# Optimization experiments

Measured on AMD Instinct MI355X. Metric: run time of the kernel, lower is better.

## Reference

```python
import jax, jax.numpy as jnp
import numpy as np

COMM_RANGE = 0.5
PATCH = 32
B, N, C_IN, H, W = 32, 8, 3, 224, 224
C, S, HM, CO = 384, 49, 512, 256


def setup_inputs() -> dict:
    key = jax.random.key(0)
    ks = jax.random.split(key, 20)
    sc = 0.02
    return {
        "img_raw": jax.random.normal(ks[0], (B, N, C_IN, H, W), jnp.float32),
        "pos": jax.random.uniform(ks[1], (B, N, 3), jnp.float32),
        "rot": jax.random.uniform(ks[2], (B, N, 3), jnp.float32),
        "W_patch": jax.random.normal(ks[3], (C, C_IN, PATCH, PATCH), jnp.float32) * sc,
        "b_patch": jax.random.normal(ks[4], (C,), jnp.float32) * sc,
        "W1a": jax.random.normal(ks[5], (C, HM), jnp.float32) * sc,
        "W1b": jax.random.normal(ks[6], (C, HM), jnp.float32) * sc,
        "b1": jax.random.normal(ks[7], (HM,), jnp.float32) * sc,
        "W2": jax.random.normal(ks[8], (HM, CO), jnp.float32) * sc,
        "b2": jax.random.normal(ks[9], (CO,), jnp.float32) * sc,
        "Wp": jax.random.normal(ks[10], (CO, 2), jnp.float32) * sc,
        "bp": jax.random.normal(ks[11], (2,), jnp.float32) * sc,
        "Wpv": jax.random.normal(ks[12], (CO, 2), jnp.float32) * sc,
        "bpv": jax.random.normal(ks[13], (2,), jnp.float32) * sc,
        "Wr": jax.random.normal(ks[14], (CO, 2), jnp.float32) * sc,
        "br": jax.random.normal(ks[15], (2,), jnp.float32) * sc,
        "Wrv": jax.random.normal(ks[16], (CO, 1), jnp.float32) * sc,
        "brv": jax.random.normal(ks[17], (1,), jnp.float32) * sc,
    }


def reference(img_raw, pos, rot, W_patch, b_patch, W1a, W1b, b1, W2, b2,
              Wp, bp, Wpv, bpv, Wr, br, Wrv, brv):
    # enc: patch-embed all B*N node images ONCE (the original redundantly
    # re-encodes per edge; math per node is identical).
    img = img_raw.reshape(B * N, C_IN, H, W)
    x = jax.lax.conv_general_dilated(
        img, W_patch, window_strides=(PATCH, PATCH), padding='VALID',
        dimension_numbers=('NCHW', 'OIHW', 'NCHW'))          # [BN, C, 7, 7]
    feats = x.reshape(B * N, C, S).transpose(0, 2, 1) + b_patch  # [BN, S, C]
    feats = feats.reshape(B, N, S, C)

    # radius graph per batch (dense, fixed shape, masked) -- loop=False
    pos2 = pos[..., :2]                                      # [B, N, 2]
    d2 = jnp.sum((pos2[:, :, None] - pos2[:, None, :]) ** 2, axis=-1)
    mask = (d2 < COMM_RANGE ** 2) & (~jnp.eye(N, dtype=bool))  # [B, N, N]
    mf = mask.reshape(B * N * N).astype(feats.dtype)

    # msg: per-token MLP on concat(x_i, x_j); split first layer so we never
    # materialize the [B,N,N,S,2C] concat.
    a = jnp.einsum('bnsc,ch->bnsh', feats, W1a)              # receiver term
    g = jnp.einsum('bnsc,ch->bnsh', feats, W1b)              # sender term
    h = jax.nn.relu(a[:, :, None] + g[:, None, :] + b1)      # [B,N,N,S,HM]
    m = jnp.einsum('bijsh,ho->bijo', h / S, W2) + b2         # mean-pool + fc

    # post: four heads -> pos(2), pos_var(2), rot(2), rot_var(1)
    heads = jnp.concatenate(
        [m @ Wp + bp, m @ Wpv + bpv, m @ Wr + br, m @ Wrv + brv], axis=-1)
    edge_out = heads.reshape(B * N * N, 7) * mf[:, None]     # masked edges

    node_preds = jnp.zeros((B, N, 1, 60, 60), jnp.float32)
    return edge_out, mask.reshape(B * N * N), node_preds
```

## Files before the change

kernel.cpp:

```cpp
#include <hip/hip_runtime.h>
#include <hip/hip_bf16.h>

typedef __attribute__((ext_vector_type(4))) float f32x4;
typedef __attribute__((ext_vector_type(8))) short s16x8;
typedef unsigned short u16;
typedef unsigned int u32;

__device__ inline u16 f2bf(float f) {
    union { float f; u32 u; } v; v.f = f;
    u32 r = v.u + 0x7FFFu + ((v.u >> 16) & 1u);
    return (u16)(r >> 16);
}
__device__ inline float bfbits2f(u32 hi_bits) {
    union { u32 u; float f; } v; v.u = hi_bits; return v.f;
}

__global__ __launch_bounds__(256) void prep_w(
    const float* __restrict__ W_patch, u16* __restrict__ wpb,
    const float* __restrict__ W1a, const float* __restrict__ W1b,
    u16* __restrict__ w1cat,
    const float* __restrict__ W2, const float* __restrict__ b2,
    const float* __restrict__ Wp, const float* __restrict__ bp,
    const float* __restrict__ Wpv, const float* __restrict__ bpv,
    const float* __restrict__ Wr, const float* __restrict__ br,
    const float* __restrict__ Wrv, const float* __restrict__ brv,
    float* __restrict__ W2h, float* __restrict__ bias7) {
    const int NW = 147456;
    const int NC = 1024 * 384;
    const int NH = 3591;
    const int total = NW + NC + NH;
    for (int idx = blockIdx.x * 256 + threadIdx.x; idx < total; idx += 256 * 256) {
        if (idx < NW) {
            int i = idx * 8;
            s16x8 o;
#pragma unroll
            for (int q = 0; q < 8; q++) o[q] = (short)f2bf(W_patch[i + q]);
            *(s16x8*)(wpb + i) = o;
        } else if (idx < NW + NC) {
            int w = idx - NW;
            int h = w / 384, k = w - h * 384;
            float v = (h < 512) ? W1a[k * 512 + h] : W1b[k * 512 + (h - 512)];
            w1cat[w] = f2bf(v);
        } else {
            int w = idx - NW - NC;
            if (w < 3584) {
                int h = w / 7, kk = w - h * 7;
                float s = 0.f;
                for (int o = 0; o < 256; o++) {
                    float ww = (kk < 2) ? Wp[o * 2 + kk]
                             : (kk < 4) ? Wpv[o * 2 + kk - 2]
                             : (kk < 6) ? Wr[o * 2 + kk - 4]
                                        : Wrv[o];
                    s += W2[h * 256 + o] * ww;
                }
                W2h[w] = s;
            } else {
                int kk = w - 3584;
                float s = (kk < 2) ? bp[kk] : (kk < 4) ? bpv[kk - 2]
                        : (kk < 6) ? br[kk - 4] : brv[0];
                for (int o = 0; o < 256; o++) {
                    float ww = (kk < 2) ? Wp[o * 2 + kk]
                             : (kk < 4) ? Wpv[o * 2 + kk - 2]
                             : (kk < 6) ? Wr[o * 2 + kk - 4]
                                        : Wrv[o];
                    s += b2[o] * ww;
                }
                bias7[kk] = s;
            }
        }
    }
}

__global__ __launch_bounds__(256) void gemm1_im2col(
    const float* __restrict__ img, const u16* __restrict__ Bt,
    u16* __restrict__ Cb, const float* __restrict__ bias) {
    constexpr int K = 3072, N = 384;
    __shared__ __align__(16) u16 As[128 * 64];
    __shared__ __align__(16) u16 Bs[64 * 64];
    const int tid = threadIdx.x;
    const int wave = tid >> 6, lane = tid & 63;
    const int wr = wave >> 1, wc = wave & 1;
    const int row0 = blockIdx.x * 128, col0 = blockIdx.y * 64;
    const int lr = lane >> 3;
    const int lcb = (lane & 7) * 8;

    const float* abase[4];
    int arow[4];
#pragma unroll
    for (int q = 0; q < 4; q++) {
        int ch = q * 4 + wave;
        int rA = ch * 8 + lr;
        int m = row0 + rA;
        int n = m / 49, s = m - n * 49;
        int py = s / 7, px = s - py * 7;
        abase[q] = img + ((size_t)(n * 3) * 224 + py * 32) * 224 + px * 32;
        arow[q] = rA;
    }
    f32x4 acc[4][2] = {};

    for (int k0 = 0; k0 < K; k0 += 64) {
        __syncthreads();
#pragma unroll
        for (int q = 0; q < 2; q++) {
            int ch = q * 4 + wave;
            const u16* gB = Bt + (size_t)(col0 + ch * 8 + lr) * K + k0 + lcb;
            __builtin_amdgcn_global_load_lds(
                (const __attribute__((address_space(1))) unsigned int*)gB,
                (__attribute__((address_space(3))) unsigned int*)(Bs + ch * 512), 16, 0, 0);
        }
        const int k = k0 + lcb;
        const int c = k >> 10;
        const int r = (k & 1023) >> 5;
        const int cc = k & 31;
        const int koff = (c * 224 + r) * 224 + cc;
        float4 va[4], vb[4];
#pragma unroll
        for (int q = 0; q < 4; q++) {
            const float* src = abase[q] + koff;
            va[q] = *(const float4*)src;
            vb[q] = *(const float4*)(src + 4);
        }
#pragma unroll
        for (int q = 0; q < 4; q++) {
            s16x8 o;
            o[0] = (short)f2bf(va[q].x); o[1] = (short)f2bf(va[q].y);
            o[2] = (short)f2bf(va[q].z); o[3] = (short)f2bf(va[q].w);
            o[4] = (short)f2bf(vb[q].x); o[5] = (short)f2bf(vb[q].y);
            o[6] = (short)f2bf(vb[q].z); o[7] = (short)f2bf(vb[q].w);
            *(s16x8*)(As + arow[q] * 64 + lcb) = o;
        }
        __syncthreads();
#pragma unroll
        for (int kk = 0; kk < 64; kk += 32) {
            s16x8 af[4], bfr[2];
#pragma unroll
            for (int m = 0; m < 4; m++)
                af[m] = *(const s16x8*)(As + (wr * 64 + m * 16 + (lane & 15)) * 64 + kk + (lane >> 4) * 8);
#pragma unroll
            for (int n = 0; n < 2; n++)
                bfr[n] = *(const s16x8*)(Bs + (wc * 32 + n * 16 + (lane & 15)) * 64 + kk + (lane >> 4) * 8);
#pragma unroll
            for (int m = 0; m < 4; m++)
#pragma unroll
                for (int n = 0; n < 2; n++)
                    acc[m][n] = __builtin_amdgcn_mfma_f32_16x16x32_bf16(af[m], bfr[n], acc[m][n], 0, 0, 0);
        }
    }
#pragma unroll
    for (int m = 0; m < 4; m++) {
        int drow = row0 + wr * 64 + m * 16 + (lane >> 4) * 4;
#pragma unroll
        for (int n = 0; n < 2; n++) {
            int dcol = col0 + wc * 32 + n * 16 + (lane & 15);
            float bv = bias[dcol];
#pragma unroll
            for (int i = 0; i < 4; i++)
                Cb[(size_t)(drow + i) * N + dcol] = f2bf(acc[m][n][i] + bv);
        }
    }
}

template<int BM, int BN>
__global__ __launch_bounds__(256) void gemm_bt(const u16* __restrict__ A,
                                               const u16* __restrict__ Bt,
                                               u16* __restrict__ Cb,
                                               const float* __restrict__ bias,
                                               int M, int N, int K) {
    constexpr int MF = BM / 32;
    constexpr int NF = BN / 32;
    __shared__ __align__(16) u16 As[BM * 64];
    __shared__ __align__(16) u16 Bs[BN * 64];
    const int tid = threadIdx.x;
    const int wave = tid >> 6, lane = tid & 63;
    const int wr = wave >> 1, wc = wave & 1;
    const int row0 = blockIdx.x * BM, col0 = blockIdx.y * BN;
    const int lr = lane >> 3;
    const int lcb = (lane & 7) * 8;
    f32x4 acc[MF][NF] = {};

    for (int k0 = 0; k0 < K; k0 += 64) {
        __syncthreads();
#pragma unroll
        for (int q = 0; q < BM / 32; q++) {
            int ch = q * 4 + wave;
            const u16* gA = A + (size_t)(row0 + ch * 8 + lr) * K + k0 + lcb;
            __builtin_amdgcn_global_load_lds(
                (const __attribute__((address_space(1))) unsigned int*)gA,
                (__attribute__((address_space(3))) unsigned int*)(As + ch * 512), 16, 0, 0);
        }
#pragma unroll
        for (int q = 0; q < BN / 32; q++) {
            int ch = q * 4 + wave;
            const u16* gB = Bt + (size_t)(col0 + ch * 8 + lr) * K + k0 + lcb;
            __builtin_amdgcn_global_load_lds(
                (const __attribute__((address_space(1))) unsigned int*)gB,
                (__attribute__((address_space(3))) unsigned int*)(Bs + ch * 512), 16, 0, 0);
        }
        __syncthreads();
#pragma unroll
        for (int kk = 0; kk < 64; kk += 32) {
            s16x8 af[MF], bfr[NF];
#pragma unroll
            for (int m = 0; m < MF; m++)
                af[m] = *(const s16x8*)(As + (wr * (BM / 2) + m * 16 + (lane & 15)) * 64 + kk + (lane >> 4) * 8);
#pragma unroll
            for (int n = 0; n < NF; n++)
                bfr[n] = *(const s16x8*)(Bs + (wc * (BN / 2) + n * 16 + (lane & 15)) * 64 + kk + (lane >> 4) * 8);
#pragma unroll
            for (int m = 0; m < MF; m++)
#pragma unroll
                for (int n = 0; n < NF; n++)
                    acc[m][n] = __builtin_amdgcn_mfma_f32_16x16x32_bf16(af[m], bfr[n], acc[m][n], 0, 0, 0);
        }
    }
#pragma unroll
    for (int m = 0; m < MF; m++) {
        int drow = row0 + wr * (BM / 2) + m * 16 + (lane >> 4) * 4;
#pragma unroll
        for (int n = 0; n < NF; n++) {
            int dcol = col0 + wc * (BN / 2) + n * 16 + (lane & 15);
            float bv = bias ? bias[dcol] : 0.0f;
#pragma unroll
            for (int i = 0; i < 4; i++)
                Cb[(size_t)(drow + i) * N + dcol] = f2bf(acc[m][n][i] + bv);
        }
    }
}

__global__ __launch_bounds__(256) void edge_kernel(
    const u16* __restrict__ ag, const float* __restrict__ pos,
    const float* __restrict__ b1, const float* __restrict__ W2h,
    const float* __restrict__ bias7,
    float* __restrict__ edge_out, float* __restrict__ mask_out,
    float* __restrict__ node_preds) {
    __shared__ float red[4][7];
    const int e = blockIdx.x;
    const int b = e >> 6, ij = e & 63, i = ij >> 3, j = ij & 7;
    const int t = threadIdx.x;
    for (int z = t; z < 450; z += 256) node_preds[(size_t)e * 450 + z] = 0.0f;
    const float dx = pos[(b * 8 + i) * 3 + 0] - pos[(b * 8 + j) * 3 + 0];
    const float dy = pos[(b * 8 + i) * 3 + 1] - pos[(b * 8 + j) * 3 + 1];
    const bool msk = (dx * dx + dy * dy < 0.25f) && (i != j);
    if (t == 0) mask_out[e] = msk ? 1.0f : 0.0f;
    if (!msk) {
        if (t < 7) edge_out[e * 7 + t] = 0.0f;
        return;
    }
    const int h0 = t * 2;
    const u16* arow = ag + (size_t)(b * 8 + i) * 49 * 1024 + h0;
    const u16* grow = ag + (size_t)(b * 8 + j) * 49 * 1024 + 512 + h0;
    const float b10 = b1[h0], b11 = b1[h0 + 1];
    float r0 = 0.f, r1 = 0.f;
#pragma unroll 7
    for (int s = 0; s < 49; s++) {
        u32 av = *(const u32*)(arow + (size_t)s * 1024);
        u32 gv = *(const u32*)(grow + (size_t)s * 1024);
        float a0 = bfbits2f(av << 16), a1 = bfbits2f(av & 0xFFFF0000u);
        float g0 = bfbits2f(gv << 16), g1 = bfbits2f(gv & 0xFFFF0000u);
        r0 += fmaxf(a0 + g0 + b10, 0.f);
        r1 += fmaxf(a1 + g1 + b11, 0.f);
    }
    float c[7];
#pragma unroll
    for (int k = 0; k < 7; k++)
        c[k] = r0 * W2h[h0 * 7 + k] + r1 * W2h[(h0 + 1) * 7 + k];
#pragma unroll
    for (int k = 0; k < 7; k++)
#pragma unroll
        for (int off = 32; off; off >>= 1)
            c[k] += __shfl_down(c[k], off, 64);
    const int lane = t & 63, wv = t >> 6;
    if (lane == 0)
        for (int k = 0; k < 7; k++) red[wv][k] = c[k];
    __syncthreads();
    if (t == 0)
        for (int k = 0; k < 7; k++) {
            float v = red[0][k] + red[1][k] + red[2][k] + red[3][k];
            edge_out[e * 7 + k] = v * (1.f / 49.f) + bias7[k];
        }
}

extern "C" void kernel_launch(void* const* d_in, const int* in_sizes, int n_in,
                              void* d_out, int out_size, void* d_ws, size_t ws_size,
                              hipStream_t stream) {
    const float* img    = (const float*)d_in[0];
    const float* pos    = (const float*)d_in[1];
    const float* W_patch= (const float*)d_in[3];
    const float* b_patch= (const float*)d_in[4];
    const float* W1a    = (const float*)d_in[5];
    const float* W1b    = (const float*)d_in[6];
    const float* b1     = (const float*)d_in[7];
    const float* W2     = (const float*)d_in[8];
    const float* b2     = (const float*)d_in[9];
    const float* Wp     = (const float*)d_in[10];
    const float* bp     = (const float*)d_in[11];
    const float* Wpv    = (const float*)d_in[12];
    const float* bpv    = (const float*)d_in[13];
    const float* Wr     = (const float*)d_in[14];
    const float* br     = (const float*)d_in[15];
    const float* Wrv    = (const float*)d_in[16];
    const float* brv    = (const float*)d_in[17];

    char* ws = (char*)d_ws;
    u16*   ag      = (u16*)(ws + 0);
    u16*   feats   = (u16*)(ws + 25690112);
    u16*   wpb     = (u16*)(ws + 35323904);
    u16*   w1cat   = (u16*)(ws + 37683200);
    float* W2h     = (float*)(ws + 38469632);
    float* bias7   = (float*)(ws + 38483968);

    float* edge_out   = (float*)d_out;
    float* mask_out   = edge_out + 14336;
    float* node_preds = mask_out + 2048;

    prep_w<<<256, 256, 0, stream>>>(W_patch, wpb, W1a, W1b, w1cat,
                                    W2, b2, Wp, bp, Wpv, bpv, Wr, br, Wrv, brv,
                                    W2h, bias7);

    dim3 g1(98, 6);
    gemm1_im2col<<<g1, 256, 0, stream>>>(img, wpb, feats, b_patch);
    dim3 g2(196, 8);
    gemm_bt<64, 128><<<g2, 256, 0, stream>>>(feats, w1cat, ag, nullptr, 12544, 1024, 384);

    edge_kernel<<<2048, 256, 0, stream>>>(ag, pos, b1, W2h, bias7,
                                          edge_out, mask_out, node_preds);
}
```

Measured before the change: 446.0 us.

## XOR-swizzle LDS tiles in GEMMs and reorder grid so column blocks vary fastest

Applies an XOR swizzle (column ^ (row&7)*8) to the LDS layouts of the A and B tiles in both GEMM kernels. For the global_load_lds path the swizzle is applied to the global source address, since the LDS destination is fixed per lane. This targets bank conflicts on the 16-byte MFMA fragment reads. The grid is also transposed so consecutive blocks share the same A row tile, which may improve L2 reuse of the image and feats reads.

```diff
diff --git a/kernel.cpp b/kernel.cpp
--- a/kernel.cpp
+++ b/kernel.cpp
@@ -14,6 +14,7 @@
 __device__ inline float bfbits2f(u32 hi_bits) {
     union { u32 u; float f; } v; v.u = hi_bits; return v.f;
 }
+__device__ inline int swz(int row, int col) { return col ^ ((row & 7) << 3); }
 
 __global__ __launch_bounds__(256) void prep_w(
     const float* __restrict__ W_patch, u16* __restrict__ wpb,
@@ -80,9 +81,10 @@
     const int tid = threadIdx.x;
     const int wave = tid >> 6, lane = tid & 63;
     const int wr = wave >> 1, wc = wave & 1;
-    const int row0 = blockIdx.x * 128, col0 = blockIdx.y * 64;
+    const int col0 = blockIdx.x * 64, row0 = blockIdx.y * 128;
     const int lr = lane >> 3;
     const int lcb = (lane & 7) * 8;
+    const int lcbs = ((lane & 7) ^ lr) * 8;
 
     const float* abase[4];
     int arow[4];
@@ -103,7 +105,7 @@
 #pragma unroll
         for (int q = 0; q < 2; q++) {
             int ch = q * 4 + wave;
-            const u16* gB = Bt + (size_t)(col0 + ch * 8 + lr) * K + k0 + lcb;
+            const u16* gB = Bt + (size_t)(col0 + ch * 8 + lr) * K + k0 + lcbs;
             __builtin_amdgcn_global_load_lds(
                 (const __attribute__((address_space(1))) unsigned int*)gB,
                 (__attribute__((address_space(3))) unsigned int*)(Bs + ch * 512), 16, 0, 0);
@@ -127,18 +129,23 @@
             o[2] = (short)f2bf(va[q].z); o[3] = (short)f2bf(va[q].w);
             o[4] = (short)f2bf(vb[q].x); o[5] = (short)f2bf(vb[q].y);
             o[6] = (short)f2bf(vb[q].z); o[7] = (short)f2bf(vb[q].w);
-            *(s16x8*)(As + arow[q] * 64 + lcb) = o;
+            *(s16x8*)(As + arow[q] * 64 + swz(arow[q], lcb)) = o;
         }
         __syncthreads();
 #pragma unroll
         for (int kk = 0; kk < 64; kk += 32) {
             s16x8 af[4], bfr[2];
-#pragma unroll
-            for (int m = 0; m < 4; m++)
-                af[m] = *(const s16x8*)(As + (wr * 64 + m * 16 + (lane & 15)) * 64 + kk + (lane >> 4) * 8);
-#pragma unroll
-            for (int n = 0; n < 2; n++)
-                bfr[n] = *(const s16x8*)(Bs + (wc * 32 + n * 16 + (lane & 15)) * 64 + kk + (lane >> 4) * 8);
+            const int rcol = kk + (lane >> 4) * 8;
+#pragma unroll
+            for (int m = 0; m < 4; m++) {
+                int row = wr * 64 + m * 16 + (lane & 15);
+                af[m] = *(const s16x8*)(As + row * 64 + swz(row, rcol));
+            }
+#pragma unroll
+            for (int n = 0; n < 2; n++) {
+                int row = wc * 32 + n * 16 + (lane & 15);
+                bfr[n] = *(const s16x8*)(Bs + row * 64 + swz(row, rcol));
+            }
 #pragma unroll
             for (int m = 0; m < 4; m++)
 #pragma unroll
@@ -173,9 +180,9 @@
     const int tid = threadIdx.x;
     const int wave = tid >> 6, lane = tid & 63;
     const int wr = wave >> 1, wc = wave & 1;
-    const int row0 = blockIdx.x * BM, col0 = blockIdx.y * BN;
+    const int col0 = blockIdx.x * BN, row0 = blockIdx.y * BM;
     const int lr = lane >> 3;
-    const int lcb = (lane & 7) * 8;
+    const int lcbs = ((lane & 7) ^ lr) * 8;
     f32x4 acc[MF][NF] = {};
 
     for (int k0 = 0; k0 < K; k0 += 64) {
@@ -183,7 +190,7 @@
 #pragma unroll
         for (int q = 0; q < BM / 32; q++) {
             int ch = q * 4 + wave;
-            const u16* gA = A + (size_t)(row0 + ch * 8 + lr) * K + k0 + lcb;
+            const u16* gA = A + (size_t)(row0 + ch * 8 + lr) * K + k0 + lcbs;
             __builtin_amdgcn_global_load_lds(
                 (const __attribute__((address_space(1))) unsigned int*)gA,
                 (__attribute__((address_space(3))) unsigned int*)(As + ch * 512), 16, 0, 0);
@@ -191,7 +198,7 @@
 #pragma unroll
         for (int q = 0; q < BN / 32; q++) {
             int ch = q * 4 + wave;
-            const u16* gB = Bt + (size_t)(col0 + ch * 8 + lr) * K + k0 + lcb;
+            const u16* gB = Bt + (size_t)(col0 + ch * 8 + lr) * K + k0 + lcbs;
             __builtin_amdgcn_global_load_lds(
                 (const __attribute__((address_space(1))) unsigned int*)gB,
                 (__attribute__((address_space(3))) unsigned int*)(Bs + ch * 512), 16, 0, 0);
@@ -200,12 +207,17 @@
 #pragma unroll
         for (int kk = 0; kk < 64; kk += 32) {
             s16x8 af[MF], bfr[NF];
-#pragma unroll
-            for (int m = 0; m < MF; m++)
-                af[m] = *(const s16x8*)(As + (wr * (BM / 2) + m * 16 + (lane & 15)) * 64 + kk + (lane >> 4) * 8);
-#pragma unroll
-            for (int n = 0; n < NF; n++)
-                bfr[n] = *(const s16x8*)(Bs + (wc * (BN / 2) + n * 16 + (lane & 15)) * 64 + kk + (lane >> 4) * 8);
+            const int rcol = kk + (lane >> 4) * 8;
+#pragma unroll
+            for (int m = 0; m < MF; m++) {
+                int row = wr * (BM / 2) + m * 16 + (lane & 15);
+                af[m] = *(const s16x8*)(As + row * 64 + swz(row, rcol));
+            }
+#pragma unroll
+            for (int n = 0; n < NF; n++) {
+                int row = wc * (BN / 2) + n * 16 + (lane & 15);
+                bfr[n] = *(const s16x8*)(Bs + row * 64 + swz(row, rcol));
+            }
 #pragma unroll
             for (int m = 0; m < MF; m++)
 #pragma unroll
@@ -317,9 +329,9 @@
                                     W2, b2, Wp, bp, Wpv, bpv, Wr, br, Wrv, brv,
                                     W2h, bias7);
 
-    dim3 g1(98, 6);
+    dim3 g1(6, 98);
     gemm1_im2col<<<g1, 256, 0, stream>>>(img, wpb, feats, b_patch);
-    dim3 g2(196, 8);
+    dim3 g2(8, 196);
     gemm_bt<64, 128><<<g2, 256, 0, stream>>>(feats, w1cat, ag, nullptr, 12544, 1024, 384);
 
     edge_kernel<<<2048, 256, 0, stream>>>(ag, pos, b1, W2h, bias7,
```

After: 426.4 us. 1.05x faster.
